# Optimization experiments

Measured on AMD Instinct MI355X. Metric: run time of the kernel, lower is better.

Reference implementation:

```python
import jax, jax.numpy as jnp
import numpy as np

M = 2  # sqrt(n_heads)

def setup_inputs() -> dict:
    key = jax.random.key(0)
    k1, k2, k3 = jax.random.split(key, 3)
    b, H, W, c = 8, 256, 256, 64
    x = jax.random.normal(k1, (b, H, W, c), dtype=jnp.float32)
    # 1x1 conv weights expressed as matrices: qkv [c, 3c], project [c, c]
    scale = 1.0 / np.sqrt(c)
    Wqkv = jax.random.normal(k2, (c, 3 * c), dtype=jnp.float32) * scale
    Wproj = jax.random.normal(k3, (c, c), dtype=jnp.float32) * scale
    return {"x": x, "Wqkv": Wqkv, "Wproj": Wproj}


def reference(x, Wqkv, Wproj):
    b, H, W, c = x.shape
    h, w = H // M, W // M
    temp = c ** (-0.5)  # n_features ** -0.5
    # 1x1 conv qkv projection (bias-free)
    qkv = jnp.einsum('byxc,cd->byxd', x, Wqkv)  # [b,H,W,3c]
    q, k, v = jnp.split(qkv, 3, axis=-1)

    def blk(t):
        # 'b (h m1) (w m2) c -> b (m1 m2) c (h w)'
        t = t.reshape(b, h, M, w, M, c)
        t = t.transpose(0, 2, 4, 5, 1, 3)  # b m1 m2 c h w
        return t.reshape(b, M * M, c, h * w)

    q, k, v = blk(q), blk(k), blk(v)
    # channel-attention: c x c score per block, contracted over hw
    score = jnp.einsum('bncl,bndl->bncd', q, k) * temp
    weight = jax.nn.softmax(score, axis=-1)
    out = jnp.einsum('bncd,bndl->bncl', weight, v)
    # inverse rearrange: 'b (m1 m2) c (h w) -> b (h m1) (w m2) c'
    out = out.reshape(b, M, M, c, h, w).transpose(0, 4, 1, 5, 2, 3).reshape(b, H, W, c)
    # 1x1 conv output projection
    return jnp.einsum('byxc,cd->byxd', out, Wproj)
```

## Files before the change

### kernel.cpp

```cpp
#include <hip/hip_runtime.h>

typedef float f32x4 __attribute__((ext_vector_type(4)));
typedef __bf16 bf16x8 __attribute__((ext_vector_type(8)));
typedef short s16x8 __attribute__((ext_vector_type(8)));

__device__ __forceinline__ unsigned short f2bf(float f) {
  unsigned u = __builtin_bit_cast(unsigned, f);
  return (unsigned short)((u + 0x7fffu + ((u >> 16) & 1u)) >> 16);
}
__device__ __forceinline__ float bf2f(unsigned short s) {
  unsigned u = ((unsigned)s) << 16;
  return __builtin_bit_cast(float, u);
}

#define LSTR 40

__global__ __launch_bounds__(256) void gram_kernel(const float* __restrict__ x,
                                                   float* __restrict__ G) {
  __shared__ unsigned short xsh[64 * LSTR];
  __shared__ unsigned short xsl[64 * LSTR];
  const int tid = threadIdx.x;
  const int lane = tid & 63;
  const int wave = tid >> 6;
  const int blk = blockIdx.x;
  const int chunk = blk & 31;
  const int bn = blk >> 5;
  const int b = bn >> 2;
  const int m1 = (bn >> 1) & 1;
  const int m2 = bn & 1;
  const int px0 = (tid & 15) * 2;
  const int c0 = (tid >> 4) * 4;
  const int mrow = lane & 15;
  const int k8 = (lane >> 4) * 8;
  const int tr0 = (wave >> 1) * 2;
  const int tc0 = (wave & 1) * 2;

  f32x4 acc[2][2];
#pragma unroll
  for (int i = 0; i < 2; ++i)
#pragma unroll
    for (int j = 0; j < 2; ++j) acc[i][j] = (f32x4){0.f, 0.f, 0.f, 0.f};

  for (int ks = 0; ks < 16; ++ks) {
    int l0 = chunk * 512 + ks * 32 + px0;
    int hy = l0 >> 7, wx = l0 & 127;
    int y = 2 * hy + m1, xx = 2 * wx + m2;
    const float* p0 = x + ((b * 256 + y) * 256 + xx) * 64 + c0;
    f32x4 v0 = *(const f32x4*)p0;
    f32x4 v1 = *(const f32x4*)(p0 + 128);
    __syncthreads();
#pragma unroll
    for (int i = 0; i < 4; ++i) {
      unsigned short h0 = f2bf(v0[i]), h1 = f2bf(v1[i]);
      unsigned short g0 = f2bf(v0[i] - bf2f(h0)), g1 = f2bf(v1[i] - bf2f(h1));
      *(unsigned*)&xsh[(c0 + i) * LSTR + px0] = (unsigned)h0 | ((unsigned)h1 << 16);
      *(unsigned*)&xsl[(c0 + i) * LSTR + px0] = (unsigned)g0 | ((unsigned)g1 << 16);
    }
    __syncthreads();
    s16x8 rh[2], rl[2], qh[2], ql[2];
#pragma unroll
    for (int i = 0; i < 2; ++i) {
      rh[i] = *(const s16x8*)&xsh[(16 * (tr0 + i) + mrow) * LSTR + k8];
      rl[i] = *(const s16x8*)&xsl[(16 * (tr0 + i) + mrow) * LSTR + k8];
      qh[i] = *(const s16x8*)&xsh[(16 * (tc0 + i) + mrow) * LSTR + k8];
      ql[i] = *(const s16x8*)&xsl[(16 * (tc0 + i) + mrow) * LSTR + k8];
    }
#pragma unroll
    for (int i = 0; i < 2; ++i)
#pragma unroll
      for (int j = 0; j < 2; ++j) {
        bf16x8 ah = __builtin_bit_cast(bf16x8, rh[i]);
        bf16x8 al = __builtin_bit_cast(bf16x8, rl[i]);
        bf16x8 bh = __builtin_bit_cast(bf16x8, qh[j]);
        bf16x8 bl = __builtin_bit_cast(bf16x8, ql[j]);
        acc[i][j] = __builtin_amdgcn_mfma_f32_16x16x32_bf16(ah, bh, acc[i][j], 0, 0, 0);
        acc[i][j] = __builtin_amdgcn_mfma_f32_16x16x32_bf16(ah, bl, acc[i][j], 0, 0, 0);
        acc[i][j] = __builtin_amdgcn_mfma_f32_16x16x32_bf16(al, bh, acc[i][j], 0, 0, 0);
      }
  }
  float* Gp = G + bn * 4096;
#pragma unroll
  for (int i = 0; i < 2; ++i)
#pragma unroll
    for (int j = 0; j < 2; ++j)
#pragma unroll
      for (int r = 0; r < 4; ++r) {
        int row = 16 * (tr0 + i) + (lane >> 4) * 4 + r;
        int col = 16 * (tc0 + j) + (lane & 15);
        atomicAdd(&Gp[row * 64 + col], acc[i][j][r]);
      }
}

__device__ __forceinline__ void mm64(const float* Ab, int ars, int acs,
                                     const float* Bb, float* Dst, int ds,
                                     float scale, int ti4, int tj4) {
  float acc[4][4] = {};
  for (int kk = 0; kk < 64; ++kk) {
    float av[4];
#pragma unroll
    for (int i = 0; i < 4; ++i) av[i] = Ab[(ti4 + i) * ars + kk * acs];
#pragma unroll
    for (int j = 0; j < 4; ++j) {
      float bv = Bb[kk * 68 + tj4 + j];
#pragma unroll
      for (int i = 0; i < 4; ++i) acc[i][j] += av[i] * bv;
    }
  }
#pragma unroll
  for (int i = 0; i < 4; ++i)
#pragma unroll
    for (int j = 0; j < 4; ++j) Dst[(ti4 + i) * ds + tj4 + j] = scale * acc[i][j];
}

__global__ __launch_bounds__(256) void fuse_kernel(const float* __restrict__ G,
                                                   const float* __restrict__ Wqkv,
                                                   const float* __restrict__ Wproj,
                                                   float* __restrict__ F) {
  __shared__ float A[64 * 68];
  __shared__ float B[64 * 68];
  __shared__ float T[64 * 68];
  const int tid = threadIdx.x;
  const int bn = blockIdx.x;
  const int ti4 = (tid >> 4) * 4, tj4 = (tid & 15) * 4;

  for (int i = tid; i < 4096; i += 256) {
    int r = i >> 6, c = i & 63;
    A[r * 68 + c] = G[bn * 4096 + i];
    B[r * 68 + c] = Wqkv[r * 192 + 64 + c];
  }
  __syncthreads();
  mm64(A, 68, 1, B, T, 68, 1.f, ti4, tj4);
  __syncthreads();
  for (int i = tid; i < 4096; i += 256) {
    int r = i >> 6, c = i & 63;
    B[r * 68 + c] = Wqkv[r * 192 + c];
  }
  __syncthreads();
  mm64(B, 1, 68, T, A, 68, 0.125f, ti4, tj4);
  __syncthreads();
  if (tid < 64) {
    float mx = -1e30f;
    for (int d = 0; d < 64; ++d) mx = fmaxf(mx, A[tid * 68 + d]);
    float s = 0.f;
    for (int d = 0; d < 64; ++d) {
      float e = __expf(A[tid * 68 + d] - mx);
      A[tid * 68 + d] = e;
      s += e;
    }
    float inv = 1.f / s;
    for (int d = 0; d < 64; ++d) A[tid * 68 + d] *= inv;
  }
  __syncthreads();
  for (int i = tid; i < 4096; i += 256) {
    int r = i >> 6, c = i & 63;
    B[r * 68 + c] = Wproj[i];
  }
  __syncthreads();
  mm64(A, 1, 68, B, T, 68, 1.f, ti4, tj4);
  __syncthreads();
  for (int i = tid; i < 4096; i += 256) {
    int r = i >> 6, c = i & 63;
    B[r * 68 + c] = Wqkv[r * 192 + 128 + c];
  }
  __syncthreads();
  mm64(B, 68, 1, T, F + bn * 4096, 64, 1.f, ti4, tj4);
}

__global__ __launch_bounds__(256) void out_kernel(const float* __restrict__ x,
                                                  const float* __restrict__ F,
                                                  float* __restrict__ out) {
  const int tid = threadIdx.x;
  const int lane = tid & 63;
  const int wave = tid >> 6;
  const int blk = blockIdx.x;
  const int hyg = blk & 63;
  const int bn = blk >> 6;
  const int b = bn >> 2;
  const int m1 = (bn >> 1) & 1;
  const int m2 = bn & 1;

  s16x8 bh[2][4], bl[2][4];
  const float* Fp = F + bn * 4096;
#pragma unroll
  for (int ksj = 0; ksj < 2; ++ksj)
#pragma unroll
    for (int tc = 0; tc < 4; ++tc) {
      s16x8 hv, lv;
#pragma unroll
      for (int j = 0; j < 8; ++j) {
        int k = ksj * 32 + (lane >> 4) * 8 + j;
        int e = tc * 16 + (lane & 15);
        float f = Fp[k * 64 + e];
        unsigned short hb = f2bf(f);
        hv[j] = (short)hb;
        lv[j] = (short)f2bf(f - bf2f(hb));
      }
      bh[ksj][tc] = hv;
      bl[ksj][tc] = lv;
    }

  for (int r = 0; r < 2; ++r) {
    int hy = hyg * 2 + r;
    int y = 2 * hy + m1;
    const float* xrow = x + ((b * 256 + y) * 256) * 64;
    float* orow = out + ((b * 256 + y) * 256) * 64;
#pragma unroll
    for (int ptI = 0; ptI < 2; ++ptI) {
      int pt = wave + ptI * 4;
      int wx = pt * 16 + (lane & 15);
      int xx = 2 * wx + m2;
      const float* pp = xrow + xx * 64 + (lane >> 4) * 8;
      s16x8 ah[2], al[2];
#pragma unroll
      for (int ksj = 0; ksj < 2; ++ksj) {
        f32x4 u0 = *(const f32x4*)(pp + ksj * 32);
        f32x4 u1 = *(const f32x4*)(pp + ksj * 32 + 4);
        s16x8 hv, lv;
#pragma unroll
        for (int j = 0; j < 4; ++j) {
          unsigned short hb0 = f2bf(u0[j]);
          unsigned short hb1 = f2bf(u1[j]);
          hv[j] = (short)hb0;
          hv[4 + j] = (short)hb1;
          lv[j] = (short)f2bf(u0[j] - bf2f(hb0));
          lv[4 + j] = (short)f2bf(u1[j] - bf2f(hb1));
        }
        ah[ksj] = hv;
        al[ksj] = lv;
      }
      f32x4 acc[4];
#pragma unroll
      for (int tc = 0; tc < 4; ++tc) acc[tc] = (f32x4){0.f, 0.f, 0.f, 0.f};
#pragma unroll
      for (int ksj = 0; ksj < 2; ++ksj)
#pragma unroll
        for (int tc = 0; tc < 4; ++tc) {
          bf16x8 A_h = __builtin_bit_cast(bf16x8, ah[ksj]);
          bf16x8 A_l = __builtin_bit_cast(bf16x8, al[ksj]);
          bf16x8 B_h = __builtin_bit_cast(bf16x8, bh[ksj][tc]);
          bf16x8 B_l = __builtin_bit_cast(bf16x8, bl[ksj][tc]);
          acc[tc] = __builtin_amdgcn_mfma_f32_16x16x32_bf16(A_h, B_h, acc[tc], 0, 0, 0);
          acc[tc] = __builtin_amdgcn_mfma_f32_16x16x32_bf16(A_h, B_l, acc[tc], 0, 0, 0);
          acc[tc] = __builtin_amdgcn_mfma_f32_16x16x32_bf16(A_l, B_h, acc[tc], 0, 0, 0);
        }
#pragma unroll
      for (int tc = 0; tc < 4; ++tc)
#pragma unroll
        for (int j = 0; j < 4; ++j) {
          int prow = (lane >> 4) * 4 + j;
          int xx2 = 2 * (pt * 16 + prow) + m2;
          orow[xx2 * 64 + tc * 16 + (lane & 15)] = acc[tc][j];
        }
    }
  }
}

extern "C" void kernel_launch(void* const* d_in, const int* in_sizes, int n_in,
                              void* d_out, int out_size, void* d_ws, size_t ws_size,
                              hipStream_t stream) {
  (void)in_sizes; (void)n_in; (void)out_size; (void)ws_size;
  const float* x = (const float*)d_in[0];
  const float* Wqkv = (const float*)d_in[1];
  const float* Wproj = (const float*)d_in[2];
  float* out = (float*)d_out;
  float* G = (float*)d_ws;
  float* F = G + 32 * 4096;

  hipMemsetAsync(G, 0, 32 * 4096 * sizeof(float), stream);
  gram_kernel<<<1024, 256, 0, stream>>>(x, G);
  fuse_kernel<<<32, 256, 0, stream>>>(G, Wqkv, Wproj, F);
  out_kernel<<<2048, 256, 0, stream>>>(x, F, out);
}
```

Measured before the change: 285.2 us.

## Replace gram atomics with partial sums, double-buffer gram LDS, vectorize fuse kernel

Each gram block now writes its own partial 64x64 Gram tile to workspace instead of atomically adding into a shared buffer. This drops the memset and the atomic contention, and the fuse kernel sums the partials. The gram loop double-buffers LDS and prefetches the next global load into registers, so there is one barrier per step instead of two. The fuse kernel's small matmuls, weight loads and softmax are vectorized with float4 and use a wave-shuffle softmax. The output kernel uses nontemporal stores. The cost is extra workspace traffic for the partials, and the chunk count drops if the workspace is too small.

```diff
diff --git a/kernel.cpp b/kernel.cpp
--- a/kernel.cpp
+++ b/kernel.cpp
@@ -16,15 +16,17 @@
 #define LSTR 40
 
 __global__ __launch_bounds__(256) void gram_kernel(const float* __restrict__ x,
-                                                   float* __restrict__ G) {
-  __shared__ unsigned short xsh[64 * LSTR];
-  __shared__ unsigned short xsl[64 * LSTR];
+                                                   float* __restrict__ Gpart,
+                                                   int shift, int steps) {
+  __shared__ __align__(16) unsigned short xsh[2][64 * LSTR];
+  __shared__ __align__(16) unsigned short xsl[2][64 * LSTR];
   const int tid = threadIdx.x;
   const int lane = tid & 63;
   const int wave = tid >> 6;
   const int blk = blockIdx.x;
-  const int chunk = blk & 31;
-  const int bn = blk >> 5;
+  const int nchm1 = (1 << shift) - 1;
+  const int chunk = blk & nchm1;
+  const int bn = blk >> shift;
   const int b = bn >> 2;
   const int m1 = (bn >> 1) & 1;
   const int m2 = bn & 1;
@@ -41,29 +43,40 @@
 #pragma unroll
     for (int j = 0; j < 2; ++j) acc[i][j] = (f32x4){0.f, 0.f, 0.f, 0.f};
 
-  for (int ks = 0; ks < 16; ++ks) {
-    int l0 = chunk * 512 + ks * 32 + px0;
+  const int l0base = chunk * steps * 32 + px0;
+  auto addr = [&](int ks) {
+    int l0 = l0base + ks * 32;
     int hy = l0 >> 7, wx = l0 & 127;
     int y = 2 * hy + m1, xx = 2 * wx + m2;
-    const float* p0 = x + ((b * 256 + y) * 256 + xx) * 64 + c0;
-    f32x4 v0 = *(const f32x4*)p0;
-    f32x4 v1 = *(const f32x4*)(p0 + 128);
-    __syncthreads();
+    return x + ((b * 256 + y) * 256 + xx) * 64 + c0;
+  };
+
+  const float* p0 = addr(0);
+  f32x4 v0 = *(const f32x4*)p0;
+  f32x4 v1 = *(const f32x4*)(p0 + 128);
+  int pb = 0;
+
+  for (int ks = 0; ks < steps; ++ks) {
 #pragma unroll
     for (int i = 0; i < 4; ++i) {
       unsigned short h0 = f2bf(v0[i]), h1 = f2bf(v1[i]);
       unsigned short g0 = f2bf(v0[i] - bf2f(h0)), g1 = f2bf(v1[i] - bf2f(h1));
-      *(unsigned*)&xsh[(c0 + i) * LSTR + px0] = (unsigned)h0 | ((unsigned)h1 << 16);
-      *(unsigned*)&xsl[(c0 + i) * LSTR + px0] = (unsigned)g0 | ((unsigned)g1 << 16);
+      *(unsigned*)&xsh[pb][(c0 + i) * LSTR + px0] = (unsigned)h0 | ((unsigned)h1 << 16);
+      *(unsigned*)&xsl[pb][(c0 + i) * LSTR + px0] = (unsigned)g0 | ((unsigned)g1 << 16);
     }
     __syncthreads();
+    if (ks + 1 < steps) {
+      const float* pn = addr(ks + 1);
+      v0 = *(const f32x4*)pn;
+      v1 = *(const f32x4*)(pn + 128);
+    }
     s16x8 rh[2], rl[2], qh[2], ql[2];
 #pragma unroll
     for (int i = 0; i < 2; ++i) {
-      rh[i] = *(const s16x8*)&xsh[(16 * (tr0 + i) + mrow) * LSTR + k8];
-      rl[i] = *(const s16x8*)&xsl[(16 * (tr0 + i) + mrow) * LSTR + k8];
-      qh[i] = *(const s16x8*)&xsh[(16 * (tc0 + i) + mrow) * LSTR + k8];
-      ql[i] = *(const s16x8*)&xsl[(16 * (tc0 + i) + mrow) * LSTR + k8];
+      rh[i] = *(const s16x8*)&xsh[pb][(16 * (tr0 + i) + mrow) * LSTR + k8];
+      rl[i] = *(const s16x8*)&xsl[pb][(16 * (tr0 + i) + mrow) * LSTR + k8];
+      qh[i] = *(const s16x8*)&xsh[pb][(16 * (tc0 + i) + mrow) * LSTR + k8];
+      ql[i] = *(const s16x8*)&xsl[pb][(16 * (tc0 + i) + mrow) * LSTR + k8];
     }
 #pragma unroll
     for (int i = 0; i < 2; ++i)
@@ -77,8 +90,9 @@
         acc[i][j] = __builtin_amdgcn_mfma_f32_16x16x32_bf16(ah, bl, acc[i][j], 0, 0, 0);
         acc[i][j] = __builtin_amdgcn_mfma_f32_16x16x32_bf16(al, bh, acc[i][j], 0, 0, 0);
       }
-  }
-  float* Gp = G + bn * 4096;
+    pb ^= 1;
+  }
+  float* Gp = Gpart + (((size_t)bn << shift) + chunk) * 4096;
 #pragma unroll
   for (int i = 0; i < 2; ++i)
 #pragma unroll
@@ -87,83 +101,127 @@
       for (int r = 0; r < 4; ++r) {
         int row = 16 * (tr0 + i) + (lane >> 4) * 4 + r;
         int col = 16 * (tc0 + j) + (lane & 15);
-        atomicAdd(&Gp[row * 64 + col], acc[i][j][r]);
-      }
-}
-
-__device__ __forceinline__ void mm64(const float* Ab, int ars, int acs,
-                                     const float* Bb, float* Dst, int ds,
-                                     float scale, int ti4, int tj4) {
+        Gp[row * 64 + col] = acc[i][j][r];
+      }
+}
+
+__device__ __forceinline__ void mm_colA(const float* Ab, const float* Bb,
+                                        float* Dst, float scale, int ti4, int tj4) {
   float acc[4][4] = {};
+#pragma unroll 8
   for (int kk = 0; kk < 64; ++kk) {
-    float av[4];
-#pragma unroll
-    for (int i = 0; i < 4; ++i) av[i] = Ab[(ti4 + i) * ars + kk * acs];
-#pragma unroll
-    for (int j = 0; j < 4; ++j) {
-      float bv = Bb[kk * 68 + tj4 + j];
-#pragma unroll
-      for (int i = 0; i < 4; ++i) acc[i][j] += av[i] * bv;
-    }
-  }
-#pragma unroll
-  for (int i = 0; i < 4; ++i)
-#pragma unroll
-    for (int j = 0; j < 4; ++j) Dst[(ti4 + i) * ds + tj4 + j] = scale * acc[i][j];
-}
-
-__global__ __launch_bounds__(256) void fuse_kernel(const float* __restrict__ G,
+    f32x4 a = *(const f32x4*)&Ab[kk * 68 + ti4];
+    f32x4 b = *(const f32x4*)&Bb[kk * 68 + tj4];
+#pragma unroll
+    for (int i = 0; i < 4; ++i)
+#pragma unroll
+      for (int j = 0; j < 4; ++j) acc[i][j] += a[i] * b[j];
+  }
+#pragma unroll
+  for (int i = 0; i < 4; ++i) {
+    f32x4 o = {acc[i][0] * scale, acc[i][1] * scale, acc[i][2] * scale, acc[i][3] * scale};
+    *(f32x4*)&Dst[(ti4 + i) * 68 + tj4] = o;
+  }
+}
+
+__device__ __forceinline__ void mm_rowA(const float* Ab, const float* Bb,
+                                        float* Dst, int ti4, int tj4) {
+  float acc[4][4] = {};
+#pragma unroll 2
+  for (int kk0 = 0; kk0 < 64; kk0 += 4) {
+    f32x4 a4[4], b4[4];
+#pragma unroll
+    for (int i = 0; i < 4; ++i) a4[i] = *(const f32x4*)&Ab[(ti4 + i) * 68 + kk0];
+#pragma unroll
+    for (int kx = 0; kx < 4; ++kx) b4[kx] = *(const f32x4*)&Bb[(kk0 + kx) * 68 + tj4];
+#pragma unroll
+    for (int kx = 0; kx < 4; ++kx)
+#pragma unroll
+      for (int i = 0; i < 4; ++i)
+#pragma unroll
+        for (int j = 0; j < 4; ++j) acc[i][j] += a4[i][kx] * b4[kx][j];
+  }
+#pragma unroll
+  for (int i = 0; i < 4; ++i) {
+    f32x4 o = {acc[i][0], acc[i][1], acc[i][2], acc[i][3]};
+    *(f32x4*)&Dst[(ti4 + i) * 64 + tj4] = o;
+  }
+}
+
+__device__ __forceinline__ void loadW(float* Bsh, const float* W, int ldw, int off, int tid) {
+  for (int i = tid * 4; i < 4096; i += 1024) {
+    int r = i >> 6, c = i & 63;
+    *(f32x4*)&Bsh[r * 68 + c] = *(const f32x4*)&W[r * ldw + off + c];
+  }
+}
+
+__global__ __launch_bounds__(256) void fuse_kernel(const float* __restrict__ Gpart,
                                                    const float* __restrict__ Wqkv,
                                                    const float* __restrict__ Wproj,
-                                                   float* __restrict__ F) {
-  __shared__ float A[64 * 68];
-  __shared__ float B[64 * 68];
-  __shared__ float T[64 * 68];
+                                                   float* __restrict__ F, int nch) {
+  __shared__ __align__(16) float A[64 * 68];
+  __shared__ __align__(16) float B[64 * 68];
+  __shared__ __align__(16) float T[64 * 68];
   const int tid = threadIdx.x;
   const int bn = blockIdx.x;
   const int ti4 = (tid >> 4) * 4, tj4 = (tid & 15) * 4;
 
-  for (int i = tid; i < 4096; i += 256) {
-    int r = i >> 6, c = i & 63;
-    A[r * 68 + c] = G[bn * 4096 + i];
-    B[r * 68 + c] = Wqkv[r * 192 + 64 + c];
-  }
-  __syncthreads();
-  mm64(A, 68, 1, B, T, 68, 1.f, ti4, tj4);
-  __syncthreads();
-  for (int i = tid; i < 4096; i += 256) {
-    int r = i >> 6, c = i & 63;
-    B[r * 68 + c] = Wqkv[r * 192 + c];
-  }
-  __syncthreads();
-  mm64(B, 1, 68, T, A, 68, 0.125f, ti4, tj4);
-  __syncthreads();
-  if (tid < 64) {
+  {
+    const float* gp = Gpart + (size_t)bn * nch * 4096;
+    for (int i = tid * 4; i < 4096; i += 1024) {
+      f32x4 s = {0.f, 0.f, 0.f, 0.f};
+      for (int p = 0; p < nch; ++p) s += *(const f32x4*)&gp[p * 4096 + i];
+      int r = i >> 6, c = i & 63;
+      *(f32x4*)&A[r * 68 + c] = s;
+      *(f32x4*)&B[r * 68 + c] = *(const f32x4*)&Wqkv[r * 192 + 64 + c];
+    }
+  }
+  __syncthreads();
+  mm_colA(A, B, T, 1.f, ti4, tj4);
+  __syncthreads();
+  loadW(B, Wqkv, 192, 0, tid);
+  __syncthreads();
+  mm_colA(B, T, A, 0.125f, ti4, tj4);
+  __syncthreads();
+  {
+    const int row = tid >> 2, q = tid & 3;
+    float* Ar = A + row * 68 + q * 16;
+    f32x4 v[4];
+#pragma unroll
+    for (int t = 0; t < 4; ++t) v[t] = *(const f32x4*)&Ar[t * 4];
     float mx = -1e30f;
-    for (int d = 0; d < 64; ++d) mx = fmaxf(mx, A[tid * 68 + d]);
+#pragma unroll
+    for (int t = 0; t < 4; ++t)
+#pragma unroll
+      for (int e = 0; e < 4; ++e) mx = fmaxf(mx, v[t][e]);
+    mx = fmaxf(mx, __shfl_xor(mx, 1));
+    mx = fmaxf(mx, __shfl_xor(mx, 2));
     float s = 0.f;
-    for (int d = 0; d < 64; ++d) {
-      float e = __expf(A[tid * 68 + d] - mx);
-      A[tid * 68 + d] = e;
-      s += e;
-    }
+#pragma unroll
+    for (int t = 0; t < 4; ++t)
+#pragma unroll
+      for (int e = 0; e < 4; ++e) {
+        float ev = __expf(v[t][e] - mx);
+        v[t][e] = ev;
+        s += ev;
+      }
+    s += __shfl_xor(s, 1);
+    s += __shfl_xor(s, 2);
     float inv = 1.f / s;
-    for (int d = 0; d < 64; ++d) A[tid * 68 + d] *= inv;
-  }
-  __syncthreads();
-  for (int i = tid; i < 4096; i += 256) {
-    int r = i >> 6, c = i & 63;
-    B[r * 68 + c] = Wproj[i];
-  }
-  __syncthreads();
-  mm64(A, 1, 68, B, T, 68, 1.f, ti4, tj4);
-  __syncthreads();
-  for (int i = tid; i < 4096; i += 256) {
-    int r = i >> 6, c = i & 63;
-    B[r * 68 + c] = Wqkv[r * 192 + 128 + c];
-  }
-  __syncthreads();
-  mm64(B, 68, 1, T, F + bn * 4096, 64, 1.f, ti4, tj4);
+#pragma unroll
+    for (int t = 0; t < 4; ++t) {
+      v[t] *= inv;
+      *(f32x4*)&Ar[t * 4] = v[t];
+    }
+  }
+  __syncthreads();
+  loadW(B, Wproj, 64, 0, tid);
+  __syncthreads();
+  mm_colA(A, B, T, 1.f, ti4, tj4);
+  __syncthreads();
+  loadW(B, Wqkv, 192, 128, tid);
+  __syncthreads();
+  mm_rowA(B, T, F + bn * 4096, ti4, tj4);
 }
 
 __global__ __launch_bounds__(256) void out_kernel(const float* __restrict__ x,
@@ -249,7 +307,7 @@
         for (int j = 0; j < 4; ++j) {
           int prow = (lane >> 4) * 4 + j;
           int xx2 = 2 * (pt * 16 + prow) + m2;
-          orow[xx2 * 64 + tc * 16 + (lane & 15)] = acc[tc][j];
+          __builtin_nontemporal_store(acc[tc][j], &orow[xx2 * 64 + tc * 16 + (lane & 15)]);
         }
     }
   }
@@ -258,16 +316,25 @@
 extern "C" void kernel_launch(void* const* d_in, const int* in_sizes, int n_in,
                               void* d_out, int out_size, void* d_ws, size_t ws_size,
                               hipStream_t stream) {
-  (void)in_sizes; (void)n_in; (void)out_size; (void)ws_size;
+  (void)in_sizes; (void)n_in; (void)out_size;
   const float* x = (const float*)d_in[0];
   const float* Wqkv = (const float*)d_in[1];
   const float* Wproj = (const float*)d_in[2];
   float* out = (float*)d_out;
-  float* G = (float*)d_ws;
-  float* F = G + 32 * 4096;
-
-  hipMemsetAsync(G, 0, 32 * 4096 * sizeof(float), stream);
-  gram_kernel<<<1024, 256, 0, stream>>>(x, G);
-  fuse_kernel<<<32, 256, 0, stream>>>(G, Wqkv, Wproj, F);
+
+  int shift = 5;
+  while (shift > 0) {
+    size_t need = ((32ull << shift) + 32ull) * 4096ull * 4ull;
+    if (need <= ws_size) break;
+    --shift;
+  }
+  const int nch = 1 << shift;
+  const int steps = 512 >> shift;
+
+  float* Gpart = (float*)d_ws;
+  float* F = Gpart + ((size_t)32 << shift) * 4096;
+
+  gram_kernel<<<32 * nch, 256, 0, stream>>>(x, Gpart, shift, steps);
+  fuse_kernel<<<32, 256, 0, stream>>>(Gpart, Wqkv, Wproj, F, nch);
   out_kernel<<<2048, 256, 0, stream>>>(x, F, out);
 }
```

Measured after the change: 309.3 us. 1.08x slower.
